# Kernel optimization log

Measured on AMD Instinct MI355X. Metric: run time of the kernel, lower is better.

Reference implementation:

```python
import jax, jax.numpy as jnp
import numpy as np

HIDDEN = 512
NUM_LAYERS = 2


def _lstm_dir(x, Wi, Wh, b, reverse):
    """Single-direction LSTM over x: [B, T, D] -> [B, T, H].

    Faithful to flax nn.LSTMCell: gates i,f,g,o where input projection has no
    bias and hidden projection carries the bias; new_c = f*c + i*g,
    new_h = o*tanh(new_c). Input projection is batched over all timesteps.
    """
    B = x.shape[0]
    H = Wh.shape[0]
    # Precompute input-to-hidden for every step: [T, B, 4H]
    xw = jnp.einsum('btd,dg->tbg', x, Wi) + b
    c0 = jnp.zeros((B, H), x.dtype)
    h0 = jnp.zeros((B, H), x.dtype)

    def step(carry, xt):
        c, h = carry
        z = xt + h @ Wh  # [B, 4H]
        i, f, g, o = jnp.split(z, 4, axis=-1)
        i = jax.nn.sigmoid(i)
        f = jax.nn.sigmoid(f)
        g = jnp.tanh(g)
        o = jax.nn.sigmoid(o)
        c = f * c + i * g
        h = o * jnp.tanh(c)
        return (c, h), h

    _, ys = jax.lax.scan(step, (c0, h0), xw, reverse=reverse)
    return jnp.transpose(ys, (1, 0, 2))  # [B, T, H]


def _bilstm(x, params):
    hidden = x
    for l in range(NUM_LAYERS):
        Wi_f, Wh_f, b_f, Wi_b, Wh_b, b_b = params[l]
        h_fwd = _lstm_dir(hidden, Wi_f, Wh_f, b_f, reverse=False)
        h_bwd = _lstm_dir(hidden, Wi_b, Wh_b, b_b, reverse=True)
        hidden = jnp.concatenate([h_fwd, h_bwd], axis=-1)
        # dropout is identity in eval (deterministic) mode
    return hidden


def setup_inputs() -> dict:
    key = jax.random.key(0)
    B, T, D, H = 32, 512, 256, HIDDEN
    ks = jax.random.split(key, 1 + 6 * NUM_LAYERS)
    x = jax.random.normal(ks[0], (B, T, D), dtype=jnp.float32)
    inp = {"x": x}
    kidx = 1
    in_dim = D
    for l in range(NUM_LAYERS):
        for d in ("f", "b"):
            inp[f"Wi_{d}{l}"] = jax.random.normal(ks[kidx], (in_dim, 4 * H), jnp.float32) * 0.05; kidx += 1
            inp[f"Wh_{d}{l}"] = jax.random.normal(ks[kidx], (H, 4 * H), jnp.float32) * 0.05; kidx += 1
            inp[f"b_{d}{l}"] = jax.random.normal(ks[kidx], (4 * H,), jnp.float32) * 0.05; kidx += 1
        in_dim = 2 * H
    return inp


def reference(x, Wi_f0, Wh_f0, b_f0, Wi_b0, Wh_b0, b_b0,
              Wi_f1, Wh_f1, b_f1, Wi_b1, Wh_b1, b_b1):
    params = [
        (Wi_f0, Wh_f0, b_f0, Wi_b0, Wh_b0, b_b0),
        (Wi_f1, Wh_f1, b_f1, Wi_b1, Wh_b1, b_b1),
    ]
    return _bilstm(x, params)
```

## Files before the change

### kernel.cpp

```cpp
#include <hip/hip_runtime.h>
#include <stdint.h>

#define TSTEPS 512
#define BATCH  32
#define HID    512
#define G4     2048
#define OUTW   1024
#define MTOT   (TSTEPS * BATCH)

#define NBLK   16
#define KROW   528
#define HSZ    (64 * KROW)
#define ZLBYTES (128 * 33 * 4)

typedef __attribute__((ext_vector_type(8))) short bf16x8;
typedef __attribute__((ext_vector_type(4))) float f32x4;

__device__ __forceinline__ float sigf(float x) { return 1.0f / (1.0f + __expf(-x)); }
__device__ __forceinline__ float tanhf_fast(float x) { return 2.0f / (1.0f + __expf(-2.0f * x)) - 1.0f; }

__device__ __forceinline__ unsigned short f2bf(float f) {
    unsigned int u = __float_as_uint(f);
    u += 0x7fffu + ((u >> 16) & 1u);
    return (unsigned short)(u >> 16);
}
__device__ __forceinline__ float bf2f(unsigned short u) {
    return __uint_as_float((unsigned int)u << 16);
}
__device__ __forceinline__ void addxw(f32x4& a, uint2 u) {
    a.x += bf2f((unsigned short)(u.x & 0xffff));
    a.y += bf2f((unsigned short)(u.x >> 16));
    a.z += bf2f((unsigned short)(u.y & 0xffff));
    a.w += bf2f((unsigned short)(u.y >> 16));
}

__global__ __launch_bounds__(256) void gemm_xw_mfma(
    const float* __restrict__ X, int K,
    const float* __restrict__ W,
    const float* __restrict__ bias,
    unsigned short* __restrict__ XWt)
{
    extern __shared__ char gsm[];
    char* Abuf = gsm;
    char* Bbuf = gsm + 18432;

    const int tid = threadIdx.x;
    const int n0 = blockIdx.x * 128;
    const int m0 = blockIdx.y * 128;
    const int w  = tid >> 6;
    const int l  = tid & 63;
    const int lc16 = l & 15;
    const int lq4  = l >> 4;
    const int wr = w >> 1, wc = w & 1;

    const int ar  = tid >> 1;
    const int akh = tid & 1;
    const int mg  = m0 + ar;
    const float* aptr = X + (size_t)(mg & 31) * ((size_t)TSTEPS * K)
                          + (size_t)(mg >> 5) * K + akh * 16;
    const int bnp = tid & 63;
    const int bkg = tid >> 6;
    const float* bptr = W + n0 + bnp * 2;

    f32x4 acc[4][4];
    #pragma unroll
    for (int i = 0; i < 4; ++i)
        #pragma unroll
        for (int j = 0; j < 4; ++j) acc[i][j] = (f32x4){0.f, 0.f, 0.f, 0.f};

    const int KT = K >> 5;
    float4 a0, a1, a2, a3;
    float2 bw[8];

#define GLOADS(KT0) do { \
    const float* ap = aptr + (KT0) * 32; \
    a0 = *(const float4*)(ap);      a1 = *(const float4*)(ap + 4); \
    a2 = *(const float4*)(ap + 8);  a3 = *(const float4*)(ap + 12); \
    _Pragma("unroll") \
    for (int i = 0; i < 8; ++i) \
        bw[i] = *(const float2*)(bptr + (size_t)((KT0) * 32 + bkg * 8 + i) * G4); \
} while (0)

    GLOADS(0);

    for (int kt = 0; kt < KT; ++kt) {
        __syncthreads();
        {
            float av[16] = {a0.x,a0.y,a0.z,a0.w, a1.x,a1.y,a1.z,a1.w,
                            a2.x,a2.y,a2.z,a2.w, a3.x,a3.y,a3.z,a3.w};
            bf16x8 h0, h1, l0, l1;
            #pragma unroll
            for (int i = 0; i < 8; ++i) {
                unsigned short hh = f2bf(av[i]);
                h0[i] = (short)hh; l0[i] = (short)f2bf(av[i] - bf2f(hh));
                unsigned short hh2 = f2bf(av[i + 8]);
                h1[i] = (short)hh2; l1[i] = (short)f2bf(av[i + 8] - bf2f(hh2));
            }
            char* ab = Abuf + ar * 144 + akh * 32;
            *(bf16x8*)(ab)      = h0;
            *(bf16x8*)(ab + 16) = h1;
            *(bf16x8*)(ab + 64) = l0;
            *(bf16x8*)(ab + 80) = l1;
        }
        {
            bf16x8 bh[2], bl[2];
            #pragma unroll
            for (int c = 0; c < 2; ++c) {
                #pragma unroll
                for (int i = 0; i < 8; ++i) {
                    float v = c ? bw[i].y : bw[i].x;
                    unsigned short hh = f2bf(v);
                    bh[c][i] = (short)hh;
                    bl[c][i] = (short)f2bf(v - bf2f(hh));
                }
                char* bb = Bbuf + (bnp * 2 + c) * 144 + bkg * 16;
                *(bf16x8*)(bb)      = bh[c];
                *(bf16x8*)(bb + 64) = bl[c];
            }
        }
        __syncthreads();
        if (kt + 1 < KT) GLOADS(kt + 1);

        bf16x8 ah[4], al[4], bh[4], bl[4];
        #pragma unroll
        for (int rt = 0; rt < 4; ++rt) {
            const char* ab = Abuf + (wr * 64 + rt * 16 + lc16) * 144 + lq4 * 16;
            ah[rt] = *(const bf16x8*)(ab);
            al[rt] = *(const bf16x8*)(ab + 64);
        }
        #pragma unroll
        for (int ct = 0; ct < 4; ++ct) {
            const char* bb = Bbuf + (wc * 64 + ct * 16 + lc16) * 144 + lq4 * 16;
            bh[ct] = *(const bf16x8*)(bb);
            bl[ct] = *(const bf16x8*)(bb + 64);
        }
        #pragma unroll
        for (int rt = 0; rt < 4; ++rt)
            #pragma unroll
            for (int ct = 0; ct < 4; ++ct) {
                acc[rt][ct] = __builtin_amdgcn_mfma_f32_16x16x32_bf16(ah[rt], bh[ct], acc[rt][ct], 0, 0, 0);
                acc[rt][ct] = __builtin_amdgcn_mfma_f32_16x16x32_bf16(al[rt], bh[ct], acc[rt][ct], 0, 0, 0);
                acc[rt][ct] = __builtin_amdgcn_mfma_f32_16x16x32_bf16(ah[rt], bl[ct], acc[rt][ct], 0, 0, 0);
            }
    }
#undef GLOADS

    #pragma unroll
    for (int ct = 0; ct < 4; ++ct) {
        const int n = n0 + wc * 64 + ct * 16 + lc16;
        const float bn = bias[n];
        #pragma unroll
        for (int rt = 0; rt < 4; ++rt) {
            const int m = m0 + wr * 64 + rt * 16 + lq4 * 4;
            f32x4 v = acc[rt][ct];
            uint2 pk;
            pk.x = (unsigned)f2bf(v.x + bn) | ((unsigned)f2bf(v.y + bn) << 16);
            pk.y = (unsigned)f2bf(v.z + bn) | ((unsigned)f2bf(v.w + bn) << 16);
            *(uint2*)(XWt + (size_t)n * MTOT + m) = pk;
        }
    }
}

__global__ __launch_bounds__(256, 1) void lstm_scan11(
    const unsigned short* __restrict__ xw_f,
    const unsigned short* __restrict__ xw_b,
    const float* __restrict__ Wh_f,
    const float* __restrict__ Wh_b,
    float* __restrict__ out,
    unsigned short* __restrict__ hbuf,
    int* __restrict__ flags,
    int lval)
{
    extern __shared__ char smem[];
    float* ZL = (float*)(smem + HSZ);

    const int tid  = threadIdx.x;
    const int l    = tid & 63;
    const int w    = tid >> 6;
    const int dir  = blockIdx.x & 1;
    const int P    = blockIdx.x >> 1;
    const int p_eff = P * 4 + w;
    const int lc16 = l & 15;
    const int lq4  = l >> 4;

    const unsigned short* __restrict__ xw = dir ? xw_b : xw_f;
    const float* __restrict__ Wh = dir ? Wh_b : Wh_f;
    char* hb  = (char*)hbuf + (size_t)dir * 65536;
    int*  flg = flags + dir * TSTEPS * 16;

    bf16x8 wfh[16][2], wfl[16][2];
    #pragma unroll
    for (int ki = 0; ki < 16; ++ki) {
        #pragma unroll
        for (int ct = 0; ct < 2; ++ct) {
            const int zc  = ct * 16 + lc16;
            const int col = p_eff * 8 + (zc & 7) + 512 * (zc >> 3);
            const float* src = Wh + (size_t)(ki * 32 + lq4 * 8) * G4 + col;
            bf16x8 vh, vl;
            #pragma unroll
            for (int r = 0; r < 8; ++r) {
                float v = src[(size_t)r * G4];
                unsigned short h16 = f2bf(v);
                vh[r] = (short)h16;
                vl[r] = (short)f2bf(v - bf2f(h16));
            }
            wfh[ki][ct] = vh;
            wfl[ki][ct] = vl;
        }
    }

    const int gc0 = p_eff * 8 + (lc16 & 7) + 512 * (lc16 >> 3);
    const unsigned short* xc0 = xw + (size_t)gc0 * MTOT;
    const unsigned short* xc1 = xw + (size_t)(gc0 + 1024) * MTOT;

    const int gb = tid & 31;
    const int jg = tid >> 5;
    float* outg = out + (size_t)gb * TSTEPS * OUTW + dir * HID + P * 32 + jg * 4;
    float cq[4] = {0.f, 0.f, 0.f, 0.f};

    for (int s = 0; s < TSTEPS; ++s) {
        const int t = dir ? (TSTEPS - 1 - s) : s;

        const int xoff = t * 32 + lq4 * 4;
        uint2 u00 = *(const uint2*)(xc0 + xoff);
        uint2 u10 = *(const uint2*)(xc0 + xoff + 16);
        uint2 u01 = *(const uint2*)(xc1 + xoff);
        uint2 u11 = *(const uint2*)(xc1 + xoff + 16);

        f32x4 acc00 = {0,0,0,0}, acc01 = {0,0,0,0}, acc10 = {0,0,0,0}, acc11 = {0,0,0,0};

        if (s > 0) {
            if (w == 0) {
                const int* fp = &flg[(s - 1) * 16 + (l & 15)];
                int fv;
                do {
                    asm volatile("global_load_dword %0, %1, off sc0 sc1\n\t"
                                 "s_waitcnt vmcnt(0)"
                                 : "=v"(fv) : "v"(fp) : "memory");
                } while (__any(fv != lval));
            }
            __syncthreads();

            const char* hsrc = hb + ((s - 1) & 1) * 32768;
            float4 rg[8];
            #pragma unroll
            for (int c = 0; c < 8; ++c) {
                const char* sp = hsrc + c * 4096 + tid * 16;
                asm volatile("global_load_dwordx4 %0, %1, off sc0 sc1"
                             : "=v"(rg[c]) : "v"(sp) : "memory");
            }
#define STG_WRITE(C0) do { \
            _Pragma("unroll") \
            for (int c = (C0); c < (C0) + 4; ++c) { \
                const int ip  = c * 4096 + tid * 16; \
                const int Pq  = ip >> 11; \
                const int b   = (ip >> 6) & 31; \
                const int jb  = ip & 63; \
                *(float4*)(smem + (Pq * 4 + (jb >> 4)) * KROW + b * 16) = rg[c]; \
            } } while (0)
            asm volatile("s_waitcnt vmcnt(4)" ::: "memory");
            __builtin_amdgcn_sched_barrier(0);
            STG_WRITE(0);
            asm volatile("s_waitcnt vmcnt(0)" ::: "memory");
            __builtin_amdgcn_sched_barrier(0);
            STG_WRITE(4);
#undef STG_WRITE
            __syncthreads();

            #pragma unroll
            for (int ki = 0; ki < 16; ++ki) {
                const char* ra = smem + (ki * 4 + lq4) * KROW + lc16 * 16;
                bf16x8 ah0 = *(const bf16x8*)ra;
                bf16x8 ah1 = *(const bf16x8*)(ra + 256);
                acc00 = __builtin_amdgcn_mfma_f32_16x16x32_bf16(ah0, wfh[ki][0], acc00, 0, 0, 0);
                acc10 = __builtin_amdgcn_mfma_f32_16x16x32_bf16(ah1, wfh[ki][0], acc10, 0, 0, 0);
                acc01 = __builtin_amdgcn_mfma_f32_16x16x32_bf16(ah0, wfh[ki][1], acc01, 0, 0, 0);
                acc11 = __builtin_amdgcn_mfma_f32_16x16x32_bf16(ah1, wfh[ki][1], acc11, 0, 0, 0);
                acc00 = __builtin_amdgcn_mfma_f32_16x16x32_bf16(ah0, wfl[ki][0], acc00, 0, 0, 0);
                acc10 = __builtin_amdgcn_mfma_f32_16x16x32_bf16(ah1, wfl[ki][0], acc10, 0, 0, 0);
                acc01 = __builtin_amdgcn_mfma_f32_16x16x32_bf16(ah0, wfl[ki][1], acc01, 0, 0, 0);
                acc11 = __builtin_amdgcn_mfma_f32_16x16x32_bf16(ah1, wfl[ki][1], acc11, 0, 0, 0);
            }
        } else {
            __syncthreads();
        }

        addxw(acc00, u00); addxw(acc10, u10);
        addxw(acc01, u01); addxw(acc11, u11);

        {
            const int cb = w * 32 + lc16;
            const int r0 = lq4 * 4;
            #pragma unroll
            for (int i = 0; i < 4; ++i) {
                ZL[cb * 33 + r0 + i]             = acc00[i];
                ZL[cb * 33 + 16 + r0 + i]        = acc10[i];
                ZL[(cb + 16) * 33 + r0 + i]      = acc01[i];
                ZL[(cb + 16) * 33 + 16 + r0 + i] = acc11[i];
            }
        }
        __syncthreads();

        float hv[4];
        #pragma unroll
        for (int q = 0; q < 4; ++q) {
            const int j  = jg * 4 + q;
            const int wv = j >> 3;
            const int jj = j & 7;
            const int zb = wv * 32;
            float zi = ZL[(zb + jj) * 33 + gb];
            float zf = ZL[(zb + 8 + jj) * 33 + gb];
            float zg = ZL[(zb + 16 + jj) * 33 + gb];
            float zo = ZL[(zb + 24 + jj) * 33 + gb];
            float ig = sigf(zi);
            float fg = sigf(zf);
            float gg = tanhf_fast(zg);
            float og = sigf(zo);
            cq[q] = fmaf(fg, cq[q], ig * gg);
            hv[q] = og * tanhf_fast(cq[q]);
        }

        {
            unsigned short h0 = f2bf(hv[0]), h1 = f2bf(hv[1]);
            unsigned short h2 = f2bf(hv[2]), h3 = f2bf(hv[3]);
            uint2 hi_pk;
            hi_pk.x = (unsigned)h0 | ((unsigned)h1 << 16);
            hi_pk.y = (unsigned)h2 | ((unsigned)h3 << 16);
            char* wp = hb + (s & 1) * 32768 + P * 2048 + gb * 64 + jg * 8;
            asm volatile("global_store_dwordx2 %0, %1, off sc0 sc1"
                         :: "v"(wp), "v"(hi_pk) : "memory");
        }
        asm volatile("s_waitcnt vmcnt(0)" ::: "memory");
        __syncthreads();
        if (tid == 0) {
            int* fp = &flg[s * 16 + P];
            asm volatile("global_store_dword %0, %1, off sc0 sc1"
                         :: "v"(fp), "v"(lval) : "memory");
        }
        float4 ov; ov.x = hv[0]; ov.y = hv[1]; ov.z = hv[2]; ov.w = hv[3];
        *(float4*)&outg[(size_t)t * OUTW] = ov;
    }
}

extern "C" void kernel_launch(void* const* d_in, const int* in_sizes, int n_in,
                              void* d_out, int out_size, void* d_ws, size_t ws_size,
                              hipStream_t stream)
{
    const float* x     = (const float*)d_in[0];
    const float* Wi_f0 = (const float*)d_in[1];
    const float* Wh_f0 = (const float*)d_in[2];
    const float* b_f0  = (const float*)d_in[3];
    const float* Wi_b0 = (const float*)d_in[4];
    const float* Wh_b0 = (const float*)d_in[5];
    const float* b_b0  = (const float*)d_in[6];
    const float* Wi_f1 = (const float*)d_in[7];
    const float* Wh_f1 = (const float*)d_in[8];
    const float* b_b1_unused = nullptr; (void)b_b1_unused;
    const float* b_f1  = (const float*)d_in[9];
    const float* Wi_b1 = (const float*)d_in[10];
    const float* Wh_b1 = (const float*)d_in[11];
    const float* b_b1  = (const float*)d_in[12];
    float* out = (float*)d_out;

    const size_t xw_elems = (size_t)MTOT * G4;
    unsigned short* xwf = (unsigned short*)d_ws;
    unsigned short* xwb = xwf + xw_elems;
    char* tail = (char*)d_ws + 2 * xw_elems * sizeof(unsigned short);
    unsigned short* hbuf = (unsigned short*)tail;
    int* flags = (int*)(tail + 262144);

    (void)hipMemsetAsync(flags, 0, 2 * TSTEPS * 16 * sizeof(int), stream);

    dim3 ggrid(G4 / 128, MTOT / 128);
    dim3 gblock(256);
    const size_t gsmem = 36864;
    dim3 sgrid(2 * NBLK);
    dim3 sblock(256);
    const size_t ssmem = HSZ + ZLBYTES;

    gemm_xw_mfma<<<ggrid, gblock, gsmem, stream>>>(x, 256, Wi_f0, b_f0, xwf);
    gemm_xw_mfma<<<ggrid, gblock, gsmem, stream>>>(x, 256, Wi_b0, b_b0, xwb);
    lstm_scan11<<<sgrid, sblock, ssmem, stream>>>(xwf, xwb, Wh_f0, Wh_b0, out,
                                                  hbuf, flags, 1);
    gemm_xw_mfma<<<ggrid, gblock, gsmem, stream>>>(out, 1024, Wi_f1, b_f1, xwf);
    gemm_xw_mfma<<<ggrid, gblock, gsmem, stream>>>(out, 1024, Wi_b1, b_b1, xwb);
    lstm_scan11<<<sgrid, sblock, ssmem, stream>>>(xwf, xwb, Wh_f1, Wh_b1, out,
                                                  hbuf, flags, 2);
}
```

Baseline: 5.324 ms.

## Pin each scan direction to one XCD and relax cache scope for h exchange

Launches 256 blocks and has each block read its XCC_ID, count ranks per XCD, and let the last arriver pick two XCDs with at least 16 resident blocks. Each scan direction is then placed entirely on one XCD, and the other blocks exit. When this placement succeeds, the per-step hidden-state exchange uses loads and stores scoped to the XCD's shared L2 instead of system-coherent sc0 sc1 accesses, which should cut the latency of the cross-block dependency every timestep. It adds a startup election with atomics and spin-waits plus extra idle blocks. It falls back to the old device-wide coherent scheme when no two XCDs have 16 resident blocks. Correctness relies on the assumption that all blocks of a direction share one L2.

```diff
diff --git a/kernel.cpp b/kernel.cpp
--- a/kernel.cpp
+++ b/kernel.cpp
@@ -8,13 +8,14 @@
 #define OUTW   1024
 #define MTOT   (TSTEPS * BATCH)
 
-#define NBLK   16
 #define KROW   528
 #define HSZ    (64 * KROW)
 #define ZLBYTES (128 * 33 * 4)
 
 typedef __attribute__((ext_vector_type(8))) short bf16x8;
 typedef __attribute__((ext_vector_type(4))) float f32x4;
+
+struct ScanCtl { int xcd[8]; int g; int w; int dec; int pad[5]; };
 
 __device__ __forceinline__ float sigf(float x) { return 1.0f / (1.0f + __expf(-x)); }
 __device__ __forceinline__ float tanhf_fast(float x) { return 2.0f / (1.0f + __expf(-2.0f * x)) - 1.0f; }
@@ -161,15 +162,12 @@
     }
 }
 
-__global__ __launch_bounds__(256, 1) void lstm_scan11(
-    const unsigned short* __restrict__ xw_f,
-    const unsigned short* __restrict__ xw_b,
-    const float* __restrict__ Wh_f,
-    const float* __restrict__ Wh_b,
+template <bool FAST>
+__device__ void run_scan(
+    const unsigned short* __restrict__ xw,
+    const float* __restrict__ Wh,
     float* __restrict__ out,
-    unsigned short* __restrict__ hbuf,
-    int* __restrict__ flags,
-    int lval)
+    char* hb, int* flg, int lval, int dir, int P)
 {
     extern __shared__ char smem[];
     float* ZL = (float*)(smem + HSZ);
@@ -177,16 +175,9 @@
     const int tid  = threadIdx.x;
     const int l    = tid & 63;
     const int w    = tid >> 6;
-    const int dir  = blockIdx.x & 1;
-    const int P    = blockIdx.x >> 1;
     const int p_eff = P * 4 + w;
     const int lc16 = l & 15;
     const int lq4  = l >> 4;
-
-    const unsigned short* __restrict__ xw = dir ? xw_b : xw_f;
-    const float* __restrict__ Wh = dir ? Wh_b : Wh_f;
-    char* hb  = (char*)hbuf + (size_t)dir * 65536;
-    int*  flg = flags + dir * TSTEPS * 16;
 
     bf16x8 wfh[16][2], wfl[16][2];
     #pragma unroll
@@ -246,8 +237,12 @@
             #pragma unroll
             for (int c = 0; c < 8; ++c) {
                 const char* sp = hsrc + c * 4096 + tid * 16;
-                asm volatile("global_load_dwordx4 %0, %1, off sc0 sc1"
-                             : "=v"(rg[c]) : "v"(sp) : "memory");
+                if constexpr (FAST)
+                    asm volatile("global_load_dwordx4 %0, %1, off sc0"
+                                 : "=v"(rg[c]) : "v"(sp) : "memory");
+                else
+                    asm volatile("global_load_dwordx4 %0, %1, off sc0 sc1"
+                                 : "=v"(rg[c]) : "v"(sp) : "memory");
             }
 #define STG_WRITE(C0) do { \
             _Pragma("unroll") \
@@ -327,8 +322,12 @@
             hi_pk.x = (unsigned)h0 | ((unsigned)h1 << 16);
             hi_pk.y = (unsigned)h2 | ((unsigned)h3 << 16);
             char* wp = hb + (s & 1) * 32768 + P * 2048 + gb * 64 + jg * 8;
-            asm volatile("global_store_dwordx2 %0, %1, off sc0 sc1"
-                         :: "v"(wp), "v"(hi_pk) : "memory");
+            if constexpr (FAST)
+                asm volatile("global_store_dwordx2 %0, %1, off"
+                             :: "v"(wp), "v"(hi_pk) : "memory");
+            else
+                asm volatile("global_store_dwordx2 %0, %1, off sc0 sc1"
+                             :: "v"(wp), "v"(hi_pk) : "memory");
         }
         asm volatile("s_waitcnt vmcnt(0)" ::: "memory");
         __syncthreads();
@@ -340,6 +339,80 @@
         float4 ov; ov.x = hv[0]; ov.y = hv[1]; ov.z = hv[2]; ov.w = hv[3];
         *(float4*)&outg[(size_t)t * OUTW] = ov;
     }
+}
+
+__global__ __launch_bounds__(256, 1) void lstm_scan13(
+    const unsigned short* __restrict__ xw_f,
+    const unsigned short* __restrict__ xw_b,
+    const float* __restrict__ Wh_f,
+    const float* __restrict__ Wh_b,
+    float* __restrict__ out,
+    unsigned short* __restrict__ hbuf,
+    int* __restrict__ flags,
+    ScanCtl* __restrict__ ctl,
+    int lval)
+{
+    extern __shared__ char smem[];
+    int* sh = (int*)smem;
+    const int tid = threadIdx.x;
+
+    if (tid == 0) {
+        int xcc = 0;
+        asm volatile("s_getreg_b32 %0, hwreg(HW_REG_XCC_ID)" : "=s"(xcc));
+        xcc &= 7;
+        int rank = atomicAdd(&ctl->xcd[xcc], 1);
+        asm volatile("s_waitcnt vmcnt(0)" ::: "memory");
+        int gold = atomicAdd(&ctl->g, 1);
+        asm volatile("s_waitcnt vmcnt(0)" ::: "memory");
+        if (gold == 255) {
+            int c[8];
+            #pragma unroll
+            for (int i = 0; i < 8; ++i)
+                asm volatile("global_load_dword %0, %1, off sc0 sc1\n\t"
+                             "s_waitcnt vmcnt(0)"
+                             : "=v"(c[i]) : "v"(&ctl->xcd[i]) : "memory");
+            int t0 = 0;
+            for (int i = 1; i < 8; ++i) if (c[i] > c[t0]) t0 = i;
+            int t1 = (t0 == 0) ? 1 : 0;
+            for (int i = 0; i < 8; ++i) if (i != t0 && c[i] > c[t1]) t1 = i;
+            int fast = (c[t0] >= 16 && c[t1] >= 16) ? 1 : 0;
+            int dec = 0x100 | fast | (t0 << 1) | (t1 << 4);
+            asm volatile("global_store_dword %0, %1, off sc0 sc1"
+                         :: "v"(&ctl->dec), "v"(dec) : "memory");
+        }
+        int dec;
+        do {
+            asm volatile("global_load_dword %0, %1, off sc0 sc1\n\t"
+                         "s_waitcnt vmcnt(0)"
+                         : "=v"(dec) : "v"(&ctl->dec) : "memory");
+        } while (dec == 0);
+        const int fast = dec & 1;
+        const int t0 = (dec >> 1) & 7;
+        const int t1 = (dec >> 4) & 7;
+        int dir = -1, P = -1;
+        if (fast) {
+            if (xcc == t0 && rank < 16)      { dir = 0; P = rank; }
+            else if (xcc == t1 && rank < 16) { dir = 1; P = rank; }
+        } else {
+            int wr = atomicAdd(&ctl->w, 1);
+            if (wr < 32) { dir = wr & 1; P = wr >> 1; }
+        }
+        sh[0] = fast; sh[1] = dir; sh[2] = P;
+    }
+    __syncthreads();
+    const int fast = sh[0];
+    const int dir  = sh[1];
+    const int P    = sh[2];
+    __syncthreads();
+    if (P < 0) return;
+
+    const unsigned short* xw = dir ? xw_b : xw_f;
+    const float* Wh = dir ? Wh_b : Wh_f;
+    char* hb  = (char*)hbuf + (size_t)dir * 65536;
+    int*  flg = flags + dir * TSTEPS * 16;
+
+    if (fast) run_scan<true >(xw, Wh, out, hb, flg, lval, dir, P);
+    else      run_scan<false>(xw, Wh, out, hb, flg, lval, dir, P);
 }
 
 extern "C" void kernel_launch(void* const* d_in, const int* in_sizes, int n_in,
@@ -355,7 +428,6 @@
     const float* b_b0  = (const float*)d_in[6];
     const float* Wi_f1 = (const float*)d_in[7];
     const float* Wh_f1 = (const float*)d_in[8];
-    const float* b_b1_unused = nullptr; (void)b_b1_unused;
     const float* b_f1  = (const float*)d_in[9];
     const float* Wi_b1 = (const float*)d_in[10];
     const float* Wh_b1 = (const float*)d_in[11];
@@ -368,22 +440,25 @@
     char* tail = (char*)d_ws + 2 * xw_elems * sizeof(unsigned short);
     unsigned short* hbuf = (unsigned short*)tail;
     int* flags = (int*)(tail + 262144);
-
-    (void)hipMemsetAsync(flags, 0, 2 * TSTEPS * 16 * sizeof(int), stream);
+    ScanCtl* ctl = (ScanCtl*)(tail + 262144 + 65536);
+
+    (void)hipMemsetAsync(flags, 0,
+                         2 * TSTEPS * 16 * sizeof(int) + 2 * sizeof(ScanCtl),
+                         stream);
 
     dim3 ggrid(G4 / 128, MTOT / 128);
     dim3 gblock(256);
     const size_t gsmem = 36864;
-    dim3 sgrid(2 * NBLK);
+    dim3 sgrid(256);
     dim3 sblock(256);
     const size_t ssmem = HSZ + ZLBYTES;
 
     gemm_xw_mfma<<<ggrid, gblock, gsmem, stream>>>(x, 256, Wi_f0, b_f0, xwf);
     gemm_xw_mfma<<<ggrid, gblock, gsmem, stream>>>(x, 256, Wi_b0, b_b0, xwb);
-    lstm_scan11<<<sgrid, sblock, ssmem, stream>>>(xwf, xwb, Wh_f0, Wh_b0, out,
-                                                  hbuf, flags, 1);
+    lstm_scan13<<<sgrid, sblock, ssmem, stream>>>(xwf, xwb, Wh_f0, Wh_b0, out,
+                                                  hbuf, flags, ctl + 0, 1);
     gemm_xw_mfma<<<ggrid, gblock, gsmem, stream>>>(out, 1024, Wi_f1, b_f1, xwf);
     gemm_xw_mfma<<<ggrid, gblock, gsmem, stream>>>(out, 1024, Wi_b1, b_b1, xwb);
-    lstm_scan11<<<sgrid, sblock, ssmem, stream>>>(xwf, xwb, Wh_f1, Wh_b1, out,
-                                                  hbuf, flags, 2);
-}
+    lstm_scan13<<<sgrid, sblock, ssmem, stream>>>(xwf, xwb, Wh_f1, Wh_b1, out,
+                                                  hbuf, flags, ctl + 1, 2);
+}
```

After: 4.906 ms. 1.09x faster.
